# Kernel tuning notes

Hardware: AMD Instinct MI355X
Metric: run time of the kernel (lower is better)

The kernel has to match this reference:

```python
import jax, jax.numpy as jnp
import numpy as np

OUT_DIM = 64
NUM_HEADS = 8
HID = NUM_HEADS * OUT_DIM  # 512
ALPHA = 0.01  # leaky relu slope
N_NODES = 20000
N_EDGES = 100000
MP_LEN = 3


def setup_inputs() -> dict:
    key = jax.random.key(0)
    ks = jax.random.split(key, 8)
    s = 1.0 / np.sqrt(HID)
    return {
        "features": jax.random.normal(ks[0], (N_NODES, OUT_DIM), jnp.float32),
        "W_ih": jax.random.normal(ks[1], (3 * HID, OUT_DIM), jnp.float32) * s,
        "W_hh": jax.random.normal(ks[2], (3 * HID, HID), jnp.float32) * s,
        "b_ih": jax.random.normal(ks[3], (3 * HID,), jnp.float32) * s,
        "b_hh": jax.random.normal(ks[4], (3 * HID,), jnp.float32) * s,
        "attn": jax.random.normal(ks[5], (NUM_HEADS, OUT_DIM), jnp.float32) * 0.1,
        "edge_metapath_indices": jax.random.randint(ks[6], (N_EDGES, MP_LEN), 0, N_NODES),
        "edge_dst": jax.random.randint(ks[7], (N_EDGES,), 0, N_NODES),
    }


def _gru_last_hidden(x_seq, W_ih, W_hh, b_ih, b_hh):
    """x_seq: [L, E, D] -> final hidden [E, HID] (torch nn.GRU math, h0=0)."""
    E = x_seq.shape[1]
    h0 = jnp.zeros((E, HID), x_seq.dtype)

    def step(h, x):
        gi = x @ W_ih.T + b_ih  # [E, 3*HID]
        gh = h @ W_hh.T + b_hh  # [E, 3*HID]
        i_r, i_z, i_n = jnp.split(gi, 3, axis=-1)
        h_r, h_z, h_n = jnp.split(gh, 3, axis=-1)
        r = jax.nn.sigmoid(i_r + h_r)
        z = jax.nn.sigmoid(i_z + h_z)
        n = jnp.tanh(i_n + r * h_n)
        h_new = (1.0 - z) * n + z * h
        return h_new, None

    h_last, _ = jax.lax.scan(step, h0, x_seq)
    return h_last


def reference(features, W_ih, W_hh, b_ih, b_hh, attn,
              edge_metapath_indices, edge_dst):
    N = features.shape[0]
    # gather metapath node features: [E, L, D] -> GRU over L
    edata = features[edge_metapath_indices]
    h = _gru_last_hidden(jnp.transpose(edata, (1, 0, 2)), W_ih, W_hh, b_ih, b_hh)
    eft = h.reshape(-1, NUM_HEADS, OUT_DIM)  # [E, H, D]
    # attention logits per edge/head + leaky relu
    a = jnp.sum(eft * attn[None], axis=-1)  # [E, H]
    a = jnp.where(a >= 0, a, ALPHA * a)
    # edge softmax grouped by destination node
    amax = jax.ops.segment_max(a, edge_dst, num_segments=N)  # [N, H]
    ea = jnp.exp(a - amax[edge_dst])
    denom = jax.ops.segment_sum(ea, edge_dst, num_segments=N)  # [N, H]
    alpha = ea / denom[edge_dst]  # [E, H]
    # weighted message aggregation (sum) to destination nodes
    msg = eft * alpha[:, :, None]  # [E, H, D]
    ret = jax.ops.segment_sum(msg, edge_dst, num_segments=N)  # [N, H, D]
    return ret
```

## Files before the change

kernel.cpp:

```cpp
#include <hip/hip_runtime.h>
#include <hip/hip_bf16.h>

#define N_NODES 20000
#define N_EDGES 100000
#define HID 512
#define G3 1536
#define NH 8
#define OD 64

typedef __hip_bfloat16 bf16;
typedef __attribute__((ext_vector_type(8))) short bf16x8;
typedef __attribute__((ext_vector_type(4))) float f32x4;

__device__ __forceinline__ float frcp(float x) { return __builtin_amdgcn_rcpf(x); }
__device__ __forceinline__ float fsig(float x) { return frcp(1.0f + __expf(-x)); }
__device__ __forceinline__ float ftanh(float x) { return 1.0f - 2.0f * frcp(__expf(2.0f * x) + 1.0f); }
__device__ __forceinline__ float b2f(bf16 b) { return __bfloat162float(b); }
__device__ __forceinline__ bf16 f2b(float f) { return __float2bfloat16(f); }
__device__ __forceinline__ float bs2f(short s) {
    return __uint_as_float(((unsigned)(unsigned short)s) << 16);
}
__device__ __forceinline__ float us2f(unsigned short s) {
    return __uint_as_float(((unsigned)s) << 16);
}
__device__ __forceinline__ short f2bs(float f) {
    bf16 b = __float2bfloat16(f);
    return *reinterpret_cast<short*>(&b);
}
__device__ __forceinline__ unsigned ford(float f) {
    unsigned u = __float_as_uint(f);
    return (u & 0x80000000u) ? ~u : (u | 0x80000000u);
}
__device__ __forceinline__ float iford(unsigned u) {
    return __uint_as_float((u & 0x80000000u) ? (u & 0x7fffffffu) : ~u);
}

__device__ __forceinline__ void g2l16(const void* g, void* l) {
#if __has_builtin(__builtin_amdgcn_global_load_lds)
    __builtin_amdgcn_global_load_lds((const __attribute__((address_space(1))) char*)g,
                                     (__attribute__((address_space(3))) char*)l, 16, 0, 0);
#else
    *(bf16x8*)l = *(const bf16x8*)g;
#endif
}


__global__ __launch_bounds__(256) void k_prep(const float* __restrict__ Whh,
                                              const float* __restrict__ Wih,
                                              const float* __restrict__ feat,
                                              bf16* __restrict__ WTs,
                                              bf16* __restrict__ WIE,
                                              bf16* __restrict__ featB,
                                              float* __restrict__ WIT) {
    int t = blockIdx.x * 256 + threadIdx.x;
    if (t < 98304) {
        int T = t >> 10, c = (t >> 6) & 15, l = t & 63;
        int n = T * 16 + (l & 15);
        int k = c * 32 + ((l >> 4) << 3);
        const float* src = Whh + (size_t)n * 512 + k;
        bf16x8 v;
#pragma unroll
        for (int j = 0; j < 8; ++j) v[j] = f2bs(src[j]);
        *(bf16x8*)(WTs + (size_t)t * 8) = v;
    } else if (t < 196608) {
        int u = t - 98304;
        int d = u / 1536, j = u % 1536;
        WIT[u] = Wih[(size_t)j * 64 + d];
    } else if (t < 208896) {
        int u = t - 196608;
        int l = u & 63, cc = (u >> 6) & 1, jt = (u >> 7) & 31, g = u >> 12;
        int row = g * 512 + jt * 16 + (l & 15);
        int d0 = cc * 32 + ((l >> 4) << 3);
        const float* src = Wih + (size_t)row * 64 + d0;
        bf16x8 v;
#pragma unroll
        for (int j = 0; j < 8; ++j) v[j] = f2bs(src[j]);
        *(bf16x8*)(WIE + (size_t)u * 8) = v;
    } else {
        int u = t - 208896;
        const float* src = feat + (size_t)u * 8;
        bf16x8 v;
#pragma unroll
        for (int j = 0; j < 8; ++j) v[j] = f2bs(src[j]);
        *(bf16x8*)(featB + (size_t)u * 8) = v;
    }
}

__global__ __launch_bounds__(256) void k_count(const int* __restrict__ dst,
                                               unsigned* __restrict__ cnt) {
    int e = blockIdx.x * 256 + threadIdx.x;
    if (e < N_EDGES) atomicAdd(&cnt[dst[e]], 1u);
}

#define SCAN_CH 79
__global__ __launch_bounds__(256) void k_scan(const unsigned* __restrict__ cnt,
                                              unsigned* __restrict__ base,
                                              unsigned* __restrict__ cursor) {
    __shared__ unsigned ls[256];
    int t = threadIdx.x;
    int s0 = t * SCAN_CH;
    int s1 = s0 + SCAN_CH < N_NODES ? s0 + SCAN_CH : N_NODES;
    unsigned s = 0;
    for (int i = s0; i < s1; ++i) s += cnt[i];
    ls[t] = s;
    __syncthreads();
    for (int d = 1; d < 256; d <<= 1) {
        unsigned v = (t >= d) ? ls[t - d] : 0u;
        __syncthreads();
        ls[t] += v;
        __syncthreads();
    }
    unsigned run = ls[t] - s;
    for (int i = s0; i < s1; ++i) {
        base[i] = run; cursor[i] = run; run += cnt[i];
    }
    if (t == 255) base[N_NODES] = ls[255];
}

__global__ __launch_bounds__(256) void k_fill(const int* __restrict__ dst,
                                              unsigned* __restrict__ cursor,
                                              unsigned* __restrict__ csr) {
    int e = blockIdx.x * 256 + threadIdx.x;
    if (e < N_EDGES) {
        unsigned p = atomicAdd(&cursor[dst[e]], 1u);
        csr[p] = (unsigned)e;
    }
}

__global__ __launch_bounds__(256) void k_gi(const float* __restrict__ feat,
                                            const float* __restrict__ WIT,
                                            const float* __restrict__ b_ih,
                                            const float* __restrict__ b_hh,
                                            bf16* __restrict__ G,
                                            bf16* __restrict__ H1) {
    __shared__ float fs[16][64];
    const int n0 = blockIdx.x * 16;
    const int k = blockIdx.y * 256 + threadIdx.x;
    for (int i = threadIdx.x; i < 16 * 64; i += 256)
        fs[0][i] = feat[(size_t)n0 * 64 + i];
    __syncthreads();
    float acc[3][16];
#pragma unroll
    for (int g = 0; g < 3; ++g) {
        float b = b_ih[g * 512 + k];
#pragma unroll
        for (int e = 0; e < 16; ++e) acc[g][e] = b;
    }
    for (int d = 0; d < 64; d += 4) {
        float w[3][4];
#pragma unroll
        for (int u = 0; u < 4; ++u)
#pragma unroll
            for (int g = 0; g < 3; ++g)
                w[g][u] = WIT[(size_t)(d + u) * G3 + g * 512 + k];
#pragma unroll
        for (int e = 0; e < 16; ++e) {
            float4 f = *(const float4*)&fs[e][d];
#pragma unroll
            for (int g = 0; g < 3; ++g)
                acc[g][e] += w[g][0] * f.x + w[g][1] * f.y + w[g][2] * f.z + w[g][3] * f.w;
        }
    }
    const float br = b_hh[k], bz = b_hh[512 + k], bn = b_hh[1024 + k];
#pragma unroll
    for (int e = 0; e < 16; ++e) {
        bf16* dst = G + (size_t)(n0 + e) * G3 + k * 3;
        dst[0] = f2b(acc[0][e]);
        dst[1] = f2b(acc[1][e]);
        dst[2] = f2b(acc[2][e]);
        float r1 = fsig(acc[0][e] + br);
        float z1 = fsig(acc[1][e] + bz);
        float n1 = ftanh(acc[2][e] + r1 * bn);
        H1[(size_t)(n0 + e) * HID + k] = f2b((1.0f - z1) * n1);
    }
}

__global__ __launch_bounds__(256, 2) void k_gh2(const bf16* __restrict__ H1,
                                                const bf16* __restrict__ WTs,
                                                const float* __restrict__ b_hh,
                                                bf16* __restrict__ GH2) {
    __shared__ short Bs[2][8192];
    const int tid = threadIdx.x;
    const int wave = tid >> 6, lane = tid & 63;
    const int m0 = blockIdx.x * 128;
    const int k0 = (lane >> 4) << 3;

    bf16x8 afrag[2][16];
#pragma unroll
    for (int t = 0; t < 2; ++t) {
        int row = m0 + wave * 32 + t * 16 + (lane & 15);
        int ar = row < N_NODES ? row : N_NODES - 1;
#pragma unroll
        for (int c = 0; c < 16; ++c)
            afrag[t][c] = *(const bf16x8*)(H1 + (size_t)ar * HID + c * 32 + k0);
    }

    const int col = lane & 15;
    const int qb = (lane >> 4) << 2;
    const int boff = lane * 8;

#pragma unroll
    for (int i = 0; i < 4; ++i) {
        int q = tid + i * 256;
        g2l16(WTs + (size_t)q * 8, &Bs[0][q * 8]);
    }
    __syncthreads();

    int cur = 0;
    for (int jt = 0; jt < 32; ++jt) {
        const int cj = jt * 16 + col;
        f32x4 acc[2][3];
#pragma unroll
        for (int t = 0; t < 2; ++t)
#pragma unroll
            for (int g = 0; g < 3; ++g) acc[t][g] = (f32x4){0, 0, 0, 0};
        const float br = b_hh[cj], bz = b_hh[512 + cj], bn = b_hh[1024 + cj];
        {
#pragma unroll
            for (int i = 0; i < 4; ++i) {
                int q = tid + i * 256;
                g2l16(WTs + 262144 + (size_t)jt * 8192 + q * 8, &Bs[cur ^ 1][q * 8]);
            }
            const short* cb = &Bs[cur][0];
#pragma unroll
            for (int c = 0; c < 16; ++c) {
                bf16x8 b = *(const bf16x8*)&cb[c * 512 + boff];
                acc[0][0] = __builtin_amdgcn_mfma_f32_16x16x32_bf16(afrag[0][c], b, acc[0][0], 0, 0, 0);
                acc[1][0] = __builtin_amdgcn_mfma_f32_16x16x32_bf16(afrag[1][c], b, acc[1][0], 0, 0, 0);
            }
            __syncthreads();
            cur ^= 1;
        }
        {
#pragma unroll
            for (int i = 0; i < 4; ++i) {
                int q = tid + i * 256;
                g2l16(WTs + 524288 + (size_t)jt * 8192 + q * 8, &Bs[cur ^ 1][q * 8]);
            }
            const short* cb = &Bs[cur][0];
#pragma unroll
            for (int c = 0; c < 16; ++c) {
                bf16x8 b = *(const bf16x8*)&cb[c * 512 + boff];
                acc[0][1] = __builtin_amdgcn_mfma_f32_16x16x32_bf16(afrag[0][c], b, acc[0][1], 0, 0, 0);
                acc[1][1] = __builtin_amdgcn_mfma_f32_16x16x32_bf16(afrag[1][c], b, acc[1][1], 0, 0, 0);
            }
            __syncthreads();
            cur ^= 1;
        }
        {
            if (jt < 31) {
#pragma unroll
                for (int i = 0; i < 4; ++i) {
                    int q = tid + i * 256;
                    g2l16(WTs + (size_t)(jt + 1) * 8192 + q * 8, &Bs[cur ^ 1][q * 8]);
                }
            }
            const short* cb = &Bs[cur][0];
#pragma unroll
            for (int c = 0; c < 16; ++c) {
                bf16x8 b = *(const bf16x8*)&cb[c * 512 + boff];
                acc[0][2] = __builtin_amdgcn_mfma_f32_16x16x32_bf16(afrag[0][c], b, acc[0][2], 0, 0, 0);
                acc[1][2] = __builtin_amdgcn_mfma_f32_16x16x32_bf16(afrag[1][c], b, acc[1][2], 0, 0, 0);
            }
#pragma unroll
            for (int t = 0; t < 2; ++t)
#pragma unroll
                for (int q = 0; q < 4; ++q) {
                    int e = m0 + wave * 32 + t * 16 + qb + q;
                    if (e < N_NODES) {
                        bf16* dst = GH2 + (size_t)e * G3 + cj * 3;
                        dst[0] = f2b(acc[t][0][q] + br);
                        dst[1] = f2b(acc[t][1][q] + bz);
                        dst[2] = f2b(acc[t][2][q] + bn);
                    }
                }
            __syncthreads();
            cur ^= 1;
        }
    }
}

__global__ __launch_bounds__(256) void k_h2(const bf16* __restrict__ G,
                                            const bf16* __restrict__ GH2,
                                            const bf16* __restrict__ H1,
                                            const int* __restrict__ emi,
                                            bf16* __restrict__ h2) {
    size_t i = (size_t)blockIdx.x * 256 + threadIdx.x;
    int e = (int)(i >> 6);
    int kc = (int)(i & 63) * 8;
    int i0 = emi[(size_t)e * 3 + 0];
    int i1 = emi[(size_t)e * 3 + 1];
    const bf16* g1p = G + (size_t)i1 * G3 + kc * 3;
    const bf16* ghp = GH2 + (size_t)i0 * G3 + kc * 3;
    bf16x8 h1v = *(const bf16x8*)(H1 + (size_t)i0 * HID + kc);
    short s1[24], sh[24];
    {
        bf16x8 a0 = *(const bf16x8*)g1p, a1 = *(const bf16x8*)(g1p + 8), a2 = *(const bf16x8*)(g1p + 16);
        bf16x8 c0 = *(const bf16x8*)ghp, c1 = *(const bf16x8*)(ghp + 8), c2 = *(const bf16x8*)(ghp + 16);
#pragma unroll
        for (int j = 0; j < 8; ++j) {
            s1[j] = a0[j]; s1[8 + j] = a1[j]; s1[16 + j] = a2[j];
            sh[j] = c0[j]; sh[8 + j] = c1[j]; sh[16 + j] = c2[j];
        }
    }
    bf16x8 out;
#pragma unroll
    for (int j = 0; j < 8; ++j) {
        float r = fsig(bs2f(s1[j * 3 + 0]) + bs2f(sh[j * 3 + 0]));
        float z = fsig(bs2f(s1[j * 3 + 1]) + bs2f(sh[j * 3 + 1]));
        float n = ftanh(bs2f(s1[j * 3 + 2]) + r * bs2f(sh[j * 3 + 2]));
        out[j] = f2bs((1.0f - z) * n + z * bs2f(h1v[j]));
    }
    *(bf16x8*)(h2 + (size_t)e * HID + kc) = out;
}

__global__ __launch_bounds__(256, 3) void k_gemm3(const bf16* __restrict__ featB,
                                                  const bf16* __restrict__ WTs,
                                                  const bf16* __restrict__ WIE,
                                                  const float* __restrict__ b_ih,
                                                  const float* __restrict__ b_hh,
                                                  const int* __restrict__ emi,
                                                  bf16* __restrict__ h2) {
    __shared__ short Bs[2][9216];
    __shared__ int si2[64];
    const int tid = threadIdx.x;
    const int wave = tid >> 6, lane = tid & 63;
    const int m0 = blockIdx.x * 64;
    if (tid < 64) {
        int e = m0 + tid;
        si2[tid] = emi[(size_t)(e < N_EDGES ? e : N_EDGES - 1) * 3 + 2];
    }
    const int k0 = (lane >> 4) << 3;
    const int col = lane & 15;
    const int qb = (lane >> 4) << 2;
    const int boff = lane * 8;

#pragma unroll
    for (int i = 0; i < 4; ++i) {
        int q = tid + i * 256;
        g2l16(WTs + (size_t)q * 8, &Bs[0][q * 8]);
    }
    if (tid < 128) g2l16(WIE + (size_t)tid * 8, &Bs[0][8192 + tid * 8]);
    __syncthreads();

    bf16x8 afrag[18];
    {
        int row = m0 + wave * 16 + (lane & 15);
        int ar = row < N_EDGES ? row : N_EDGES - 1;
#pragma unroll
        for (int c = 0; c < 16; ++c)
            afrag[c] = *(const bf16x8*)(h2 + (size_t)ar * HID + c * 32 + k0);
        int i2r = si2[wave * 16 + (lane & 15)];
        afrag[16] = *(const bf16x8*)(featB + (size_t)i2r * 64 + k0);
        afrag[17] = *(const bf16x8*)(featB + (size_t)i2r * 64 + 32 + k0);
    }

    int cur = 0;
    for (int jt = 0; jt < 32; ++jt) {
        const int cj = jt * 16 + col;
        f32x4 ar_ = {0, 0, 0, 0}, az_ = {0, 0, 0, 0};
        f32x4 ahn = {0, 0, 0, 0}, ain = {0, 0, 0, 0};
        float bihr, bihz, bihn, bhhr, bhhz, bhhn;
        unsigned short ph[4];
        {
            bihr = b_ih[cj]; bihz = b_ih[512 + cj]; bihn = b_ih[1024 + cj];
            bhhr = b_hh[cj]; bhhz = b_hh[512 + cj]; bhhn = b_hh[1024 + cj];
#pragma unroll
            for (int q = 0; q < 4; ++q) {
                int e = m0 + wave * 16 + qb + q;
                int ec = e < N_EDGES ? e : N_EDGES - 1;
                ph[q] = ((const unsigned short*)h2)[(size_t)ec * HID + cj];
            }
#pragma unroll
            for (int i = 0; i < 4; ++i) {
                int q = tid + i * 256;
                g2l16(WTs + 262144 + (size_t)jt * 8192 + q * 8, &Bs[cur ^ 1][q * 8]);
            }
            if (tid < 128)
                g2l16(WIE + 32768 + (size_t)jt * 1024 + tid * 8, &Bs[cur ^ 1][8192 + tid * 8]);
            const short* cb = &Bs[cur][0];
#pragma unroll
            for (int c = 0; c < 16; ++c) {
                bf16x8 b = *(const bf16x8*)&cb[c * 512 + boff];
                ar_ = __builtin_amdgcn_mfma_f32_16x16x32_bf16(afrag[c], b, ar_, 0, 0, 0);
            }
            {
                bf16x8 b16 = *(const bf16x8*)&cb[8192 + boff];
                bf16x8 b17 = *(const bf16x8*)&cb[8192 + 512 + boff];
                ar_ = __builtin_amdgcn_mfma_f32_16x16x32_bf16(afrag[16], b16, ar_, 0, 0, 0);
                ar_ = __builtin_amdgcn_mfma_f32_16x16x32_bf16(afrag[17], b17, ar_, 0, 0, 0);
            }
            __syncthreads();
            cur ^= 1;
        }
        {
#pragma unroll
            for (int i = 0; i < 4; ++i) {
                int q = tid + i * 256;
                g2l16(WTs + 524288 + (size_t)jt * 8192 + q * 8, &Bs[cur ^ 1][q * 8]);
            }
            if (tid < 128)
                g2l16(WIE + 65536 + (size_t)jt * 1024 + tid * 8, &Bs[cur ^ 1][8192 + tid * 8]);
            const short* cb = &Bs[cur][0];
#pragma unroll
            for (int c = 0; c < 16; ++c) {
                bf16x8 b = *(const bf16x8*)&cb[c * 512 + boff];
                az_ = __builtin_amdgcn_mfma_f32_16x16x32_bf16(afrag[c], b, az_, 0, 0, 0);
            }
            {
                bf16x8 b16 = *(const bf16x8*)&cb[8192 + boff];
                bf16x8 b17 = *(const bf16x8*)&cb[8192 + 512 + boff];
                az_ = __builtin_amdgcn_mfma_f32_16x16x32_bf16(afrag[16], b16, az_, 0, 0, 0);
                az_ = __builtin_amdgcn_mfma_f32_16x16x32_bf16(afrag[17], b17, az_, 0, 0, 0);
            }
            __syncthreads();
            cur ^= 1;
        }
        {
            if (jt < 31) {
#pragma unroll
                for (int i = 0; i < 4; ++i) {
                    int q = tid + i * 256;
                    g2l16(WTs + (size_t)(jt + 1) * 8192 + q * 8, &Bs[cur ^ 1][q * 8]);
                }
                if (tid < 128)
                    g2l16(WIE + (size_t)(jt + 1) * 1024 + tid * 8, &Bs[cur ^ 1][8192 + tid * 8]);
            }
            const short* cb = &Bs[cur][0];
#pragma unroll
            for (int c = 0; c < 16; ++c) {
                bf16x8 b = *(const bf16x8*)&cb[c * 512 + boff];
                ahn = __builtin_amdgcn_mfma_f32_16x16x32_bf16(afrag[c], b, ahn, 0, 0, 0);
            }
            {
                bf16x8 b16 = *(const bf16x8*)&cb[8192 + boff];
                bf16x8 b17 = *(const bf16x8*)&cb[8192 + 512 + boff];
                ain = __builtin_amdgcn_mfma_f32_16x16x32_bf16(afrag[16], b16, ain, 0, 0, 0);
                ain = __builtin_amdgcn_mfma_f32_16x16x32_bf16(afrag[17], b17, ain, 0, 0, 0);
            }
#pragma unroll
            for (int q = 0; q < 4; ++q) {
                int e = m0 + wave * 16 + qb + q;
                if (e < N_EDGES) {
                    float r = fsig(ar_[q] + bihr + bhhr);
                    float z = fsig(az_[q] + bihz + bhhz);
                    float n = ftanh(ain[q] + bihn + r * (ahn[q] + bhhn));
                    h2[(size_t)e * HID + cj] = f2b((1.0f - z) * n + z * us2f(ph[q]));
                }
            }
            __syncthreads();
            cur ^= 1;
        }
    }
}

__global__ __launch_bounds__(256) void k_logits(const bf16* __restrict__ eft,
                                                const float* __restrict__ attn,
                                                const int* __restrict__ dst,
                                                float* __restrict__ a,
                                                unsigned* __restrict__ amax) {
    int i = blockIdx.x * 256 + threadIdx.x;
    int e = i >> 3, h = i & 7;
    const __hip_bfloat162* f2 = (const __hip_bfloat162*)(eft + (size_t)e * HID + h * OD);
    const float* at = attn + h * OD;
    float s = 0.f;
#pragma unroll
    for (int d = 0; d < OD / 2; ++d) {
        float2 fv = __bfloat1622float2(f2[d]);
        s += fv.x * at[2 * d] + fv.y * at[2 * d + 1];
    }
    s = (s >= 0.f) ? s : 0.01f * s;
    a[i] = s;
    atomicMax(&amax[(size_t)dst[e] * NH + h], ford(s));
}

__global__ __launch_bounds__(256) void k_ea(const int* __restrict__ dst,
                                            const unsigned* __restrict__ amax,
                                            float* __restrict__ a,
                                            float* __restrict__ denom) {
    int i = blockIdx.x * 256 + threadIdx.x;
    int e = i >> 3, h = i & 7;
    float m = iford(amax[(size_t)dst[e] * NH + h]);
    float v = __expf(a[i] - m);
    a[i] = v;
    atomicAdd(&denom[(size_t)dst[e] * NH + h], v);
}

__global__ __launch_bounds__(256) void k_out(const bf16* __restrict__ eft,
                                             const float* __restrict__ a,
                                             const float* __restrict__ denom,
                                             const unsigned* __restrict__ base,
                                             const unsigned* __restrict__ csr,
                                             float* __restrict__ out) {
    int n = blockIdx.x;
    int k = blockIdx.y * 256 + threadIdx.x;
    int h = k >> 6;
    unsigned b0 = base[n], b1 = base[n + 1];
    float rden = (b1 > b0) ? frcp(denom[(size_t)n * NH + h]) : 0.0f;
    float acc = 0.f;
    for (unsigned i = b0; i < b1; ++i) {
        unsigned e = csr[i];
        float al = a[(size_t)e * NH + h];
        acc += b2f(eft[(size_t)e * HID + k]) * al;
    }
    out[(size_t)n * HID + k] = acc * rden;
}

extern "C" void kernel_launch(void* const* d_in, const int* in_sizes, int n_in,
                              void* d_out, int out_size, void* d_ws, size_t ws_size,
                              hipStream_t stream) {
    (void)in_sizes; (void)n_in; (void)ws_size; (void)out_size;
    const float* feat = (const float*)d_in[0];
    const float* W_ih = (const float*)d_in[1];
    const float* W_hh = (const float*)d_in[2];
    const float* b_ih = (const float*)d_in[3];
    const float* b_hh = (const float*)d_in[4];
    const float* attn = (const float*)d_in[5];
    const int* emi = (const int*)d_in[6];
    const int* dst = (const int*)d_in[7];
    float* out = (float*)d_out;

    char* ws = (char*)d_ws;
    bf16* G = (bf16*)ws;
    bf16* GH2 = (bf16*)(ws + 61440000);
    bf16* h2 = (bf16*)(ws + 122880000);
    bf16* WTs = (bf16*)(ws + 225280000);
    float* WIT = (float*)(ws + 226852864);
    float* a = (float*)(ws + 227246080);
    unsigned* amax = (unsigned*)(ws + 230446080);
    float* denom = (float*)(ws + 231086080);
    unsigned* cnt = (unsigned*)(ws + 231726080);
    unsigned* base = (unsigned*)(ws + 231806080);
    unsigned* cursor = (unsigned*)(ws + 231886088);
    unsigned* csr = (unsigned*)(ws + 231966088);
    bf16* H1 = (bf16*)(ws + 232366088);
    bf16* WIE = (bf16*)(ws + 227246080);
    bf16* featB = (bf16*)(ws + 227442688);

    (void)hipMemsetAsync(amax, 0, 1360000, stream);

    k_prep<<<1441, 256, 0, stream>>>(W_hh, W_ih, feat, WTs, WIE, featB, WIT);
    k_count<<<391, 256, 0, stream>>>(dst, cnt);
    k_scan<<<1, 256, 0, stream>>>(cnt, base, cursor);
    k_fill<<<391, 256, 0, stream>>>(dst, cursor, csr);
    k_gi<<<dim3(1250, 2), 256, 0, stream>>>(feat, WIT, b_ih, b_hh, G, H1);
    k_gh2<<<157, 256, 0, stream>>>(H1, WTs, b_hh, GH2);
    k_h2<<<25000, 256, 0, stream>>>(G, GH2, H1, emi, h2);
    k_gemm3<<<1563, 256, 0, stream>>>(featB, WTs, WIE, b_ih, b_hh, emi, h2);
    k_logits<<<3125, 256, 0, stream>>>(h2, attn, dst, a, amax);
    k_ea<<<3125, 256, 0, stream>>>(dst, amax, a, denom);
    k_out<<<dim3(N_NODES, 2), 256, 0, stream>>>(h2, a, denom, base, csr, out);
}
```

Measured before the change: 788.6 us.

## Triple-buffer gate weight tiles in GRU step-3 GEMM with explicit waitcnt pipelining

Replaces the double-buffered LDS staging in k_gemm3 with three buffers, one per gate (r, z, n). Each gate's weights are prefetched two stages ahead, and the full __syncthreads is replaced by s_waitcnt vmcnt plus s_barrier. The WIE layout is padded so every thread issues one uniform 16-byte load per stage, and s_setprio is raised around the MFMA bursts. Launch bounds drop from 3 to 2 blocks per CU to fit the larger LDS footprint, which trades occupancy for deeper prefetch.

```diff
diff --git a/kernel.cpp b/kernel.cpp
--- a/kernel.cpp
+++ b/kernel.cpp
@@ -49,7 +49,7 @@
                                               const float* __restrict__ Wih,
                                               const float* __restrict__ feat,
                                               bf16* __restrict__ WTs,
-                                              bf16* __restrict__ WIE,
+                                              bf16* __restrict__ WIEp,
                                               bf16* __restrict__ featB,
                                               float* __restrict__ WIT) {
     int t = blockIdx.x * 256 + threadIdx.x;
@@ -68,14 +68,15 @@
         WIT[u] = Wih[(size_t)j * 64 + d];
     } else if (t < 208896) {
         int u = t - 196608;
-        int l = u & 63, cc = (u >> 6) & 1, jt = (u >> 7) & 31, g = u >> 12;
+        int q = u & 127, jt = (u >> 7) & 31, g = u >> 12;
+        int l = q & 63, cc = (q >> 6) & 1;
         int row = g * 512 + jt * 16 + (l & 15);
         int d0 = cc * 32 + ((l >> 4) << 3);
         const float* src = Wih + (size_t)row * 64 + d0;
         bf16x8 v;
 #pragma unroll
         for (int j = 0; j < 8; ++j) v[j] = f2bs(src[j]);
-        *(bf16x8*)(WIE + (size_t)u * 8) = v;
+        *(bf16x8*)(WIEp + ((size_t)g * 32 + jt) * 2048 + q * 8) = v;
     } else {
         int u = t - 208896;
         const float* src = feat + (size_t)u * 8;
@@ -314,14 +315,14 @@
     *(bf16x8*)(h2 + (size_t)e * HID + kc) = out;
 }
 
-__global__ __launch_bounds__(256, 3) void k_gemm3(const bf16* __restrict__ featB,
+__global__ __launch_bounds__(256, 2) void k_gemm3(const bf16* __restrict__ featB,
                                                   const bf16* __restrict__ WTs,
-                                                  const bf16* __restrict__ WIE,
+                                                  const bf16* __restrict__ WIEp,
                                                   const float* __restrict__ b_ih,
                                                   const float* __restrict__ b_hh,
                                                   const int* __restrict__ emi,
                                                   bf16* __restrict__ h2) {
-    __shared__ short Bs[2][9216];
+    __shared__ short Bs[3][10240];
     __shared__ int si2[64];
     const int tid = threadIdx.x;
     const int wave = tid >> 6, lane = tid & 63;
@@ -335,13 +336,22 @@
     const int qb = (lane >> 4) << 2;
     const int boff = lane * 8;
 
-#pragma unroll
-    for (int i = 0; i < 4; ++i) {
-        int q = tid + i * 256;
-        g2l16(WTs + (size_t)q * 8, &Bs[0][q * 8]);
-    }
-    if (tid < 128) g2l16(WIE + (size_t)tid * 8, &Bs[0][8192 + tid * 8]);
-    __syncthreads();
+#define STAGE_G3(gg, jj, bb) do {                                                   \
+        _Pragma("unroll")                                                           \
+        for (int i_ = 0; i_ < 4; ++i_) {                                            \
+            int q_ = tid + i_ * 256;                                                \
+            g2l16(WTs + (size_t)(gg) * 262144 + (size_t)(jj) * 8192 + q_ * 8,       \
+                  &Bs[bb][q_ * 8]);                                                 \
+        }                                                                           \
+        g2l16(WIEp + ((size_t)(gg) * 32 + (jj)) * 2048 + tid * 8,                   \
+              &Bs[bb][8192 + tid * 8]);                                             \
+    } while (0)
+
+    STAGE_G3(0, 0, 0);
+    STAGE_G3(1, 0, 1);
+    asm volatile("s_waitcnt vmcnt(5) lgkmcnt(0)" ::: "memory");
+    __builtin_amdgcn_s_barrier();
+    __builtin_amdgcn_sched_barrier(0);
 
     bf16x8 afrag[18];
     {
@@ -355,7 +365,6 @@
         afrag[17] = *(const bf16x8*)(featB + (size_t)i2r * 64 + 32 + k0);
     }
 
-    int cur = 0;
     for (int jt = 0; jt < 32; ++jt) {
         const int cj = jt * 16 + col;
         f32x4 ar_ = {0, 0, 0, 0}, az_ = {0, 0, 0, 0};
@@ -363,6 +372,10 @@
         float bihr, bihz, bihn, bhhr, bhhz, bhhn;
         unsigned short ph[4];
         {
+            asm volatile("s_waitcnt vmcnt(5)" ::: "memory");
+            __builtin_amdgcn_s_barrier();
+            __builtin_amdgcn_sched_barrier(0);
+            STAGE_G3(2, jt, 2);
             bihr = b_ih[cj]; bihz = b_ih[512 + cj]; bihn = b_ih[1024 + cj];
             bhhr = b_hh[cj]; bhhz = b_hh[512 + cj]; bhhn = b_hh[1024 + cj];
 #pragma unroll
@@ -371,14 +384,8 @@
                 int ec = e < N_EDGES ? e : N_EDGES - 1;
                 ph[q] = ((const unsigned short*)h2)[(size_t)ec * HID + cj];
             }
-#pragma unroll
-            for (int i = 0; i < 4; ++i) {
-                int q = tid + i * 256;
-                g2l16(WTs + 262144 + (size_t)jt * 8192 + q * 8, &Bs[cur ^ 1][q * 8]);
-            }
-            if (tid < 128)
-                g2l16(WIE + 32768 + (size_t)jt * 1024 + tid * 8, &Bs[cur ^ 1][8192 + tid * 8]);
-            const short* cb = &Bs[cur][0];
+            const short* cb = &Bs[0][0];
+            __builtin_amdgcn_s_setprio(1);
 #pragma unroll
             for (int c = 0; c < 16; ++c) {
                 bf16x8 b = *(const bf16x8*)&cb[c * 512 + boff];
@@ -386,22 +393,19 @@
             }
             {
                 bf16x8 b16 = *(const bf16x8*)&cb[8192 + boff];
-                bf16x8 b17 = *(const bf16x8*)&cb[8192 + 512 + boff];
+                bf16x8 b17 = *(const bf16x8*)&cb[8704 + boff];
                 ar_ = __builtin_amdgcn_mfma_f32_16x16x32_bf16(afrag[16], b16, ar_, 0, 0, 0);
                 ar_ = __builtin_amdgcn_mfma_f32_16x16x32_bf16(afrag[17], b17, ar_, 0, 0, 0);
             }
-            __syncthreads();
-            cur ^= 1;
+            __builtin_amdgcn_s_setprio(0);
         }
         {
-#pragma unroll
-            for (int i = 0; i < 4; ++i) {
-                int q = tid + i * 256;
-                g2l16(WTs + 524288 + (size_t)jt * 8192 + q * 8, &Bs[cur ^ 1][q * 8]);
-            }
-            if (tid < 128)
-                g2l16(WIE + 65536 + (size_t)jt * 1024 + tid * 8, &Bs[cur ^ 1][8192 + tid * 8]);
-            const short* cb = &Bs[cur][0];
+            asm volatile("s_waitcnt vmcnt(5)" ::: "memory");
+            __builtin_amdgcn_s_barrier();
+            __builtin_amdgcn_sched_barrier(0);
+            if (jt < 31) STAGE_G3(0, jt + 1, 0);
+            const short* cb = &Bs[1][0];
+            __builtin_amdgcn_s_setprio(1);
 #pragma unroll
             for (int c = 0; c < 16; ++c) {
                 bf16x8 b = *(const bf16x8*)&cb[c * 512 + boff];
@@ -409,24 +413,23 @@
             }
             {
                 bf16x8 b16 = *(const bf16x8*)&cb[8192 + boff];
-                bf16x8 b17 = *(const bf16x8*)&cb[8192 + 512 + boff];
+                bf16x8 b17 = *(const bf16x8*)&cb[8704 + boff];
                 az_ = __builtin_amdgcn_mfma_f32_16x16x32_bf16(afrag[16], b16, az_, 0, 0, 0);
                 az_ = __builtin_amdgcn_mfma_f32_16x16x32_bf16(afrag[17], b17, az_, 0, 0, 0);
             }
-            __syncthreads();
-            cur ^= 1;
+            __builtin_amdgcn_s_setprio(0);
         }
         {
             if (jt < 31) {
-#pragma unroll
-                for (int i = 0; i < 4; ++i) {
-                    int q = tid + i * 256;
-                    g2l16(WTs + (size_t)(jt + 1) * 8192 + q * 8, &Bs[cur ^ 1][q * 8]);
-                }
-                if (tid < 128)
-                    g2l16(WIE + (size_t)(jt + 1) * 1024 + tid * 8, &Bs[cur ^ 1][8192 + tid * 8]);
-            }
-            const short* cb = &Bs[cur][0];
+                asm volatile("s_waitcnt vmcnt(5)" ::: "memory");
+            } else {
+                asm volatile("s_waitcnt vmcnt(0)" ::: "memory");
+            }
+            __builtin_amdgcn_s_barrier();
+            __builtin_amdgcn_sched_barrier(0);
+            if (jt < 31) STAGE_G3(1, jt + 1, 1);
+            const short* cb = &Bs[2][0];
+            __builtin_amdgcn_s_setprio(1);
 #pragma unroll
             for (int c = 0; c < 16; ++c) {
                 bf16x8 b = *(const bf16x8*)&cb[c * 512 + boff];
@@ -434,10 +437,11 @@
             }
             {
                 bf16x8 b16 = *(const bf16x8*)&cb[8192 + boff];
-                bf16x8 b17 = *(const bf16x8*)&cb[8192 + 512 + boff];
+                bf16x8 b17 = *(const bf16x8*)&cb[8704 + boff];
                 ain = __builtin_amdgcn_mfma_f32_16x16x32_bf16(afrag[16], b16, ain, 0, 0, 0);
                 ain = __builtin_amdgcn_mfma_f32_16x16x32_bf16(afrag[17], b17, ain, 0, 0, 0);
             }
+            __builtin_amdgcn_s_setprio(0);
 #pragma unroll
             for (int q = 0; q < 4; ++q) {
                 int e = m0 + wave * 16 + qb + q;
@@ -448,10 +452,9 @@
                     h2[(size_t)e * HID + cj] = f2b((1.0f - z) * n + z * us2f(ph[q]));
                 }
             }
-            __syncthreads();
-            cur ^= 1;
-        }
-    }
+        }
+    }
+#undef STAGE_G3
 }
 
 __global__ __launch_bounds__(256) void k_logits(const bf16* __restrict__ eft,
@@ -534,19 +537,19 @@
     unsigned* cursor = (unsigned*)(ws + 231886088);
     unsigned* csr = (unsigned*)(ws + 231966088);
     bf16* H1 = (bf16*)(ws + 232366088);
-    bf16* WIE = (bf16*)(ws + 227246080);
-    bf16* featB = (bf16*)(ws + 227442688);
+    bf16* WIEp = (bf16*)(ws + 227246080);
+    bf16* featB = (bf16*)(ws + 227639296);
 
     (void)hipMemsetAsync(amax, 0, 1360000, stream);
 
-    k_prep<<<1441, 256, 0, stream>>>(W_hh, W_ih, feat, WTs, WIE, featB, WIT);
+    k_prep<<<1441, 256, 0, stream>>>(W_hh, W_ih, feat, WTs, WIEp, featB, WIT);
     k_count<<<391, 256, 0, stream>>>(dst, cnt);
     k_scan<<<1, 256, 0, stream>>>(cnt, base, cursor);
     k_fill<<<391, 256, 0, stream>>>(dst, cursor, csr);
     k_gi<<<dim3(1250, 2), 256, 0, stream>>>(feat, WIT, b_ih, b_hh, G, H1);
     k_gh2<<<157, 256, 0, stream>>>(H1, WTs, b_hh, GH2);
     k_h2<<<25000, 256, 0, stream>>>(G, GH2, H1, emi, h2);
-    k_gemm3<<<1563, 256, 0, stream>>>(featB, WTs, WIE, b_ih, b_hh, emi, h2);
+    k_gemm3<<<1563, 256, 0, stream>>>(featB, WTs, WIEp, b_ih, b_hh, emi, h2);
     k_logits<<<3125, 256, 0, stream>>>(h2, attn, dst, a, amax);
     k_ea<<<3125, 256, 0, stream>>>(dst, amax, a, denom);
     k_out<<<dim3(N_NODES, 2), 256, 0, stream>>>(h2, a, denom, base, csr, out);
```

After: 804.5 us. 1.02x slower.

## Stage GRU output tiles in LDS for coalesced vector stores

Applied to the files above, without the earlier changes.

The GH2 kernel now collects each column tile's gate pre-activations in shared memory and writes them to global memory as 16-byte rows on the next iteration. Before this it issued scattered 2-byte stores. The final GRU step kernel loads previous-hidden tiles into LDS with async copies, updates them in place, and writes back 64-column chunks with vector stores. It also precomputes the combined biases once per block in LDS. This targets uncoalesced narrow global loads and stores, at the cost of extra LDS use, which may lower occupancy, and more synchronisation around the tile buffer.

```diff
diff --git a/kernel.cpp b/kernel.cpp
--- a/kernel.cpp
+++ b/kernel.cpp
@@ -68,7 +68,8 @@
         WIT[u] = Wih[(size_t)j * 64 + d];
     } else if (t < 208896) {
         int u = t - 196608;
-        int l = u & 63, cc = (u >> 6) & 1, jt = (u >> 7) & 31, g = u >> 12;
+        int l = u & 63, cc = (u >> 6) & 1, jg = u >> 7;
+        int jt = jg & 31, g = jg >> 5;
         int row = g * 512 + jt * 16 + (l & 15);
         int d0 = cc * 32 + ((l >> 4) << 3);
         const float* src = Wih + (size_t)row * 64 + d0;
@@ -180,6 +181,7 @@
                                                 const float* __restrict__ b_hh,
                                                 bf16* __restrict__ GH2) {
     __shared__ short Bs[2][8192];
+    __shared__ short tile2[128 * 48];
     const int tid = threadIdx.x;
     const int wave = tid >> 6, lane = tid & 63;
     const int m0 = blockIdx.x * 128;
@@ -216,6 +218,17 @@
             for (int g = 0; g < 3; ++g) acc[t][g] = (f32x4){0, 0, 0, 0};
         const float br = b_hh[cj], bz = b_hh[512 + cj], bn = b_hh[1024 + cj];
         {
+            if (jt > 0) {
+                int pj = jt - 1;
+#pragma unroll
+                for (int i_ = 0; i_ < 3; ++i_) {
+                    int idx = i_ * 256 + tid;
+                    int rg = m0 + (idx / 6);
+                    if (rg < N_NODES)
+                        *(bf16x8*)(GH2 + (size_t)rg * G3 + pj * 48 + (idx % 6) * 8) =
+                            *(const bf16x8*)&tile2[idx * 8];
+                }
+            }
 #pragma unroll
             for (int i = 0; i < 4; ++i) {
                 int q = tid + i * 256;
@@ -266,17 +279,23 @@
             for (int t = 0; t < 2; ++t)
 #pragma unroll
                 for (int q = 0; q < 4; ++q) {
-                    int e = m0 + wave * 32 + t * 16 + qb + q;
-                    if (e < N_NODES) {
-                        bf16* dst = GH2 + (size_t)e * G3 + cj * 3;
-                        dst[0] = f2b(acc[t][0][q] + br);
-                        dst[1] = f2b(acc[t][1][q] + bz);
-                        dst[2] = f2b(acc[t][2][q] + bn);
-                    }
+                    int lr = wave * 32 + t * 16 + qb + q;
+                    short* s = &tile2[lr * 48 + col * 3];
+                    s[0] = f2bs(acc[t][0][q] + br);
+                    s[1] = f2bs(acc[t][1][q] + bz);
+                    s[2] = f2bs(acc[t][2][q] + bn);
                 }
             __syncthreads();
             cur ^= 1;
         }
+    }
+#pragma unroll
+    for (int i_ = 0; i_ < 3; ++i_) {
+        int idx = i_ * 256 + tid;
+        int rg = m0 + (idx / 6);
+        if (rg < N_NODES)
+            *(bf16x8*)(GH2 + (size_t)rg * G3 + 31 * 48 + (idx % 6) * 8) =
+                *(const bf16x8*)&tile2[idx * 8];
     }
 }
 
@@ -322,6 +341,8 @@
                                                   const int* __restrict__ emi,
                                                   bf16* __restrict__ h2) {
     __shared__ short Bs[2][9216];
+    __shared__ short tile[64 * 64];
+    __shared__ float bias4[2048];
     __shared__ int si2[64];
     const int tid = threadIdx.x;
     const int wave = tid >> 6, lane = tid & 63;
@@ -330,17 +351,44 @@
         int e = m0 + tid;
         si2[tid] = emi[(size_t)(e < N_EDGES ? e : N_EDGES - 1) * 3 + 2];
     }
+#pragma unroll
+    for (int j = 0; j < 8; ++j) {
+        int idx = j * 256 + tid;
+        int arr = idx >> 9, c = idx & 511;
+        float v;
+        if (arr == 0) v = b_ih[c] + b_hh[c];
+        else if (arr == 1) v = b_ih[512 + c] + b_hh[512 + c];
+        else if (arr == 2) v = b_ih[1024 + c];
+        else v = b_hh[1024 + c];
+        bias4[idx] = v;
+    }
     const int k0 = (lane >> 4) << 3;
     const int col = lane & 15;
     const int qb = (lane >> 4) << 2;
     const int boff = lane * 8;
 
-#pragma unroll
-    for (int i = 0; i < 4; ++i) {
-        int q = tid + i * 256;
-        g2l16(WTs + (size_t)q * 8, &Bs[0][q * 8]);
-    }
-    if (tid < 128) g2l16(WIE + (size_t)tid * 8, &Bs[0][8192 + tid * 8]);
+#define STAGE_W(gg, jj) do {                                                        \
+        _Pragma("unroll")                                                           \
+        for (int i_ = 0; i_ < 4; ++i_) {                                            \
+            int q_ = tid + i_ * 256;                                                \
+            g2l16(WTs + (size_t)(gg) * 262144 + (size_t)(jj) * 8192 + q_ * 8,       \
+                  &Bs[cur ^ 1][q_ * 8]);                                            \
+        }                                                                           \
+        if (tid < 128)                                                              \
+            g2l16(WIE + (size_t)(gg) * 32768 + (size_t)(jj) * 1024 + tid * 8,       \
+                  &Bs[cur ^ 1][8192 + tid * 8]);                                    \
+    } while (0)
+
+    {
+        int cur = 1;
+        STAGE_W(0, 0);
+    }
+#pragma unroll
+    for (int i_ = 0; i_ < 2; ++i_) {
+        int idx = i_ * 256 + tid;
+        int rg = m0 + (idx >> 3); if (rg >= N_EDGES) rg = N_EDGES - 1;
+        g2l16(h2 + (size_t)rg * HID + (idx & 7) * 8, &tile[idx * 8]);
+    }
     __syncthreads();
 
     bf16x8 afrag[18];
@@ -360,24 +408,8 @@
         const int cj = jt * 16 + col;
         f32x4 ar_ = {0, 0, 0, 0}, az_ = {0, 0, 0, 0};
         f32x4 ahn = {0, 0, 0, 0}, ain = {0, 0, 0, 0};
-        float bihr, bihz, bihn, bhhr, bhhz, bhhn;
-        unsigned short ph[4];
         {
-            bihr = b_ih[cj]; bihz = b_ih[512 + cj]; bihn = b_ih[1024 + cj];
-            bhhr = b_hh[cj]; bhhz = b_hh[512 + cj]; bhhn = b_hh[1024 + cj];
-#pragma unroll
-            for (int q = 0; q < 4; ++q) {
-                int e = m0 + wave * 16 + qb + q;
-                int ec = e < N_EDGES ? e : N_EDGES - 1;
-                ph[q] = ((const unsigned short*)h2)[(size_t)ec * HID + cj];
-            }
-#pragma unroll
-            for (int i = 0; i < 4; ++i) {
-                int q = tid + i * 256;
-                g2l16(WTs + 262144 + (size_t)jt * 8192 + q * 8, &Bs[cur ^ 1][q * 8]);
-            }
-            if (tid < 128)
-                g2l16(WIE + 32768 + (size_t)jt * 1024 + tid * 8, &Bs[cur ^ 1][8192 + tid * 8]);
+            STAGE_W(1, jt);
             const short* cb = &Bs[cur][0];
 #pragma unroll
             for (int c = 0; c < 16; ++c) {
@@ -386,7 +418,7 @@
             }
             {
                 bf16x8 b16 = *(const bf16x8*)&cb[8192 + boff];
-                bf16x8 b17 = *(const bf16x8*)&cb[8192 + 512 + boff];
+                bf16x8 b17 = *(const bf16x8*)&cb[8704 + boff];
                 ar_ = __builtin_amdgcn_mfma_f32_16x16x32_bf16(afrag[16], b16, ar_, 0, 0, 0);
                 ar_ = __builtin_amdgcn_mfma_f32_16x16x32_bf16(afrag[17], b17, ar_, 0, 0, 0);
             }
@@ -394,13 +426,7 @@
             cur ^= 1;
         }
         {
-#pragma unroll
-            for (int i = 0; i < 4; ++i) {
-                int q = tid + i * 256;
-                g2l16(WTs + 524288 + (size_t)jt * 8192 + q * 8, &Bs[cur ^ 1][q * 8]);
-            }
-            if (tid < 128)
-                g2l16(WIE + 65536 + (size_t)jt * 1024 + tid * 8, &Bs[cur ^ 1][8192 + tid * 8]);
+            STAGE_W(2, jt);
             const short* cb = &Bs[cur][0];
 #pragma unroll
             for (int c = 0; c < 16; ++c) {
@@ -409,7 +435,7 @@
             }
             {
                 bf16x8 b16 = *(const bf16x8*)&cb[8192 + boff];
-                bf16x8 b17 = *(const bf16x8*)&cb[8192 + 512 + boff];
+                bf16x8 b17 = *(const bf16x8*)&cb[8704 + boff];
                 az_ = __builtin_amdgcn_mfma_f32_16x16x32_bf16(afrag[16], b16, az_, 0, 0, 0);
                 az_ = __builtin_amdgcn_mfma_f32_16x16x32_bf16(afrag[17], b17, az_, 0, 0, 0);
             }
@@ -417,15 +443,7 @@
             cur ^= 1;
         }
         {
-            if (jt < 31) {
-#pragma unroll
-                for (int i = 0; i < 4; ++i) {
-                    int q = tid + i * 256;
-                    g2l16(WTs + (size_t)(jt + 1) * 8192 + q * 8, &Bs[cur ^ 1][q * 8]);
-                }
-                if (tid < 128)
-                    g2l16(WIE + (size_t)(jt + 1) * 1024 + tid * 8, &Bs[cur ^ 1][8192 + tid * 8]);
-            }
+            if (jt < 31) STAGE_W(0, jt + 1);
             const short* cb = &Bs[cur][0];
 #pragma unroll
             for (int c = 0; c < 16; ++c) {
@@ -434,24 +452,51 @@
             }
             {
                 bf16x8 b16 = *(const bf16x8*)&cb[8192 + boff];
-                bf16x8 b17 = *(const bf16x8*)&cb[8192 + 512 + boff];
+                bf16x8 b17 = *(const bf16x8*)&cb[8704 + boff];
                 ain = __builtin_amdgcn_mfma_f32_16x16x32_bf16(afrag[16], b16, ain, 0, 0, 0);
                 ain = __builtin_amdgcn_mfma_f32_16x16x32_bf16(afrag[17], b17, ain, 0, 0, 0);
             }
-#pragma unroll
-            for (int q = 0; q < 4; ++q) {
-                int e = m0 + wave * 16 + qb + q;
-                if (e < N_EDGES) {
-                    float r = fsig(ar_[q] + bihr + bhhr);
-                    float z = fsig(az_[q] + bihz + bhhz);
-                    float n = ftanh(ain[q] + bihn + r * (ahn[q] + bhhn));
-                    h2[(size_t)e * HID + cj] = f2b((1.0f - z) * n + z * us2f(ph[q]));
+            {
+                const float rb = bias4[cj], zb = bias4[512 + cj];
+                const float nb = bias4[1024 + cj], hb = bias4[1536 + cj];
+                const int tc = ((jt & 3) << 4) + col;
+#pragma unroll
+                for (int q = 0; q < 4; ++q) {
+                    int lrow = wave * 16 + qb + q;
+                    short* slot = &tile[lrow * 64 + tc];
+                    float phv = bs2f(*slot);
+                    float r = fsig(ar_[q] + rb);
+                    float z = fsig(az_[q] + zb);
+                    float n = ftanh(ain[q] + nb + r * (ahn[q] + hb));
+                    *slot = f2bs((1.0f - z) * n + z * phv);
                 }
             }
             __syncthreads();
             cur ^= 1;
-        }
-    }
+            if ((jt & 3) == 3) {
+                const int g4 = jt >> 2;
+#pragma unroll
+                for (int i_ = 0; i_ < 2; ++i_) {
+                    int idx = i_ * 256 + tid;
+                    int rg = m0 + (idx >> 3);
+                    if (rg < N_EDGES)
+                        *(bf16x8*)(h2 + (size_t)rg * HID + g4 * 64 + (idx & 7) * 8) =
+                            *(const bf16x8*)&tile[idx * 8];
+                }
+                __builtin_amdgcn_sched_barrier(0);
+                if (jt < 31) {
+#pragma unroll
+                    for (int i_ = 0; i_ < 2; ++i_) {
+                        int idx = i_ * 256 + tid;
+                        int rg = m0 + (idx >> 3); if (rg >= N_EDGES) rg = N_EDGES - 1;
+                        g2l16(h2 + (size_t)rg * HID + (g4 + 1) * 64 + (idx & 7) * 8,
+                              &tile[idx * 8]);
+                    }
+                }
+            }
+        }
+    }
+#undef STAGE_W
 }
 
 __global__ __launch_bounds__(256) void k_logits(const bf16* __restrict__ eft,
```

Result: no change. 803.1 us (+1.8%).

## Fuse attention logits into GRU GEMM epilogue and softmax into aggregation

Applied to the files above, without the earlier changes.

Attention logit computation and the leaky-relu/atomicMax are folded into the k_gemm3 epilogue, using a per-head shuffle reduction of the hidden values times attn. The separate exp/denominator kernel is removed: k_out now recomputes exp(a-max) and the denominator on the fly while aggregating, with 512-thread blocks over the full hidden dim. k_gh2 is retiled to 64 rows per block with higher occupancy. This eliminates two launches and re-reading h2 for logits, at the cost of redundant exp work per thread in k_out and extra epilogue work in the GEMM.

```diff
diff --git a/kernel.cpp b/kernel.cpp
--- a/kernel.cpp
+++ b/kernel.cpp
@@ -68,7 +68,8 @@
         WIT[u] = Wih[(size_t)j * 64 + d];
     } else if (t < 208896) {
         int u = t - 196608;
-        int l = u & 63, cc = (u >> 6) & 1, jt = (u >> 7) & 31, g = u >> 12;
+        int l = u & 63, cc = (u >> 6) & 1, jg = u >> 7;
+        int jt = jg & 31, g = jg >> 5;
         int row = g * 512 + jt * 16 + (l & 15);
         int d0 = cc * 32 + ((l >> 4) << 3);
         const float* src = Wih + (size_t)row * 64 + d0;
@@ -175,24 +176,23 @@
     }
 }
 
-__global__ __launch_bounds__(256, 2) void k_gh2(const bf16* __restrict__ H1,
+__global__ __launch_bounds__(256, 4) void k_gh2(const bf16* __restrict__ H1,
                                                 const bf16* __restrict__ WTs,
                                                 const float* __restrict__ b_hh,
                                                 bf16* __restrict__ GH2) {
     __shared__ short Bs[2][8192];
     const int tid = threadIdx.x;
     const int wave = tid >> 6, lane = tid & 63;
-    const int m0 = blockIdx.x * 128;
+    const int m0 = blockIdx.x * 64;
     const int k0 = (lane >> 4) << 3;
 
-    bf16x8 afrag[2][16];
-#pragma unroll
-    for (int t = 0; t < 2; ++t) {
-        int row = m0 + wave * 32 + t * 16 + (lane & 15);
+    bf16x8 afrag[16];
+    {
+        int row = m0 + wave * 16 + (lane & 15);
         int ar = row < N_NODES ? row : N_NODES - 1;
 #pragma unroll
         for (int c = 0; c < 16; ++c)
-            afrag[t][c] = *(const bf16x8*)(H1 + (size_t)ar * HID + c * 32 + k0);
+            afrag[c] = *(const bf16x8*)(H1 + (size_t)ar * HID + c * 32 + k0);
     }
 
     const int col = lane & 15;
@@ -209,11 +209,7 @@
     int cur = 0;
     for (int jt = 0; jt < 32; ++jt) {
         const int cj = jt * 16 + col;
-        f32x4 acc[2][3];
-#pragma unroll
-        for (int t = 0; t < 2; ++t)
-#pragma unroll
-            for (int g = 0; g < 3; ++g) acc[t][g] = (f32x4){0, 0, 0, 0};
+        f32x4 a0 = {0, 0, 0, 0}, a1 = {0, 0, 0, 0}, a2 = {0, 0, 0, 0};
         const float br = b_hh[cj], bz = b_hh[512 + cj], bn = b_hh[1024 + cj];
         {
 #pragma unroll
@@ -225,8 +221,7 @@
 #pragma unroll
             for (int c = 0; c < 16; ++c) {
                 bf16x8 b = *(const bf16x8*)&cb[c * 512 + boff];
-                acc[0][0] = __builtin_amdgcn_mfma_f32_16x16x32_bf16(afrag[0][c], b, acc[0][0], 0, 0, 0);
-                acc[1][0] = __builtin_amdgcn_mfma_f32_16x16x32_bf16(afrag[1][c], b, acc[1][0], 0, 0, 0);
+                a0 = __builtin_amdgcn_mfma_f32_16x16x32_bf16(afrag[c], b, a0, 0, 0, 0);
             }
             __syncthreads();
             cur ^= 1;
@@ -241,8 +236,7 @@
 #pragma unroll
             for (int c = 0; c < 16; ++c) {
                 bf16x8 b = *(const bf16x8*)&cb[c * 512 + boff];
-                acc[0][1] = __builtin_amdgcn_mfma_f32_16x16x32_bf16(afrag[0][c], b, acc[0][1], 0, 0, 0);
-                acc[1][1] = __builtin_amdgcn_mfma_f32_16x16x32_bf16(afrag[1][c], b, acc[1][1], 0, 0, 0);
+                a1 = __builtin_amdgcn_mfma_f32_16x16x32_bf16(afrag[c], b, a1, 0, 0, 0);
             }
             __syncthreads();
             cur ^= 1;
@@ -259,21 +253,18 @@
 #pragma unroll
             for (int c = 0; c < 16; ++c) {
                 bf16x8 b = *(const bf16x8*)&cb[c * 512 + boff];
-                acc[0][2] = __builtin_amdgcn_mfma_f32_16x16x32_bf16(afrag[0][c], b, acc[0][2], 0, 0, 0);
-                acc[1][2] = __builtin_amdgcn_mfma_f32_16x16x32_bf16(afrag[1][c], b, acc[1][2], 0, 0, 0);
-            }
-#pragma unroll
-            for (int t = 0; t < 2; ++t)
-#pragma unroll
-                for (int q = 0; q < 4; ++q) {
-                    int e = m0 + wave * 32 + t * 16 + qb + q;
-                    if (e < N_NODES) {
-                        bf16* dst = GH2 + (size_t)e * G3 + cj * 3;
-                        dst[0] = f2b(acc[t][0][q] + br);
-                        dst[1] = f2b(acc[t][1][q] + bz);
-                        dst[2] = f2b(acc[t][2][q] + bn);
-                    }
+                a2 = __builtin_amdgcn_mfma_f32_16x16x32_bf16(afrag[c], b, a2, 0, 0, 0);
+            }
+#pragma unroll
+            for (int q = 0; q < 4; ++q) {
+                int e = m0 + wave * 16 + qb + q;
+                if (e < N_NODES) {
+                    bf16* dst = GH2 + (size_t)e * G3 + cj * 3;
+                    dst[0] = f2b(a0[q] + br);
+                    dst[1] = f2b(a1[q] + bz);
+                    dst[2] = f2b(a2[q] + bn);
                 }
+            }
             __syncthreads();
             cur ^= 1;
         }
@@ -320,16 +311,26 @@
                                                   const float* __restrict__ b_ih,
                                                   const float* __restrict__ b_hh,
                                                   const int* __restrict__ emi,
-                                                  bf16* __restrict__ h2) {
+                                                  const int* __restrict__ dst,
+                                                  const float* __restrict__ attn,
+                                                  bf16* __restrict__ h2,
+                                                  float* __restrict__ a,
+                                                  unsigned* __restrict__ amax) {
     __shared__ short Bs[2][9216];
     __shared__ int si2[64];
+    __shared__ int sdst[64];
+    __shared__ float As[512];
     const int tid = threadIdx.x;
     const int wave = tid >> 6, lane = tid & 63;
     const int m0 = blockIdx.x * 64;
     if (tid < 64) {
         int e = m0 + tid;
-        si2[tid] = emi[(size_t)(e < N_EDGES ? e : N_EDGES - 1) * 3 + 2];
-    }
+        int ec = e < N_EDGES ? e : N_EDGES - 1;
+        si2[tid] = emi[(size_t)ec * 3 + 2];
+        sdst[tid] = dst[ec];
+    }
+    As[tid] = attn[tid];
+    As[256 + tid] = attn[256 + tid];
     const int k0 = (lane >> 4) << 3;
     const int col = lane & 15;
     const int qb = (lane >> 4) << 2;
@@ -355,6 +356,7 @@
         afrag[17] = *(const bf16x8*)(featB + (size_t)i2r * 64 + 32 + k0);
     }
 
+    float hacc[4] = {0.f, 0.f, 0.f, 0.f};
     int cur = 0;
     for (int jt = 0; jt < 32; ++jt) {
         const int cj = jt * 16 + col;
@@ -438,15 +440,39 @@
                 ain = __builtin_amdgcn_mfma_f32_16x16x32_bf16(afrag[16], b16, ain, 0, 0, 0);
                 ain = __builtin_amdgcn_mfma_f32_16x16x32_bf16(afrag[17], b17, ain, 0, 0, 0);
             }
+            const float aw = As[cj];
 #pragma unroll
             for (int q = 0; q < 4; ++q) {
                 int e = m0 + wave * 16 + qb + q;
-                if (e < N_EDGES) {
-                    float r = fsig(ar_[q] + bihr + bhhr);
-                    float z = fsig(az_[q] + bihz + bhhz);
-                    float n = ftanh(ain[q] + bihn + r * (ahn[q] + bhhn));
-                    h2[(size_t)e * HID + cj] = f2b((1.0f - z) * n + z * us2f(ph[q]));
+                float r = fsig(ar_[q] + bihr + bhhr);
+                float z = fsig(az_[q] + bihz + bhhz);
+                float n = ftanh(ain[q] + bihn + r * (ahn[q] + bhhn));
+                float hv = (1.0f - z) * n + z * us2f(ph[q]);
+                hacc[q] += hv * aw;
+                if (e < N_EDGES) h2[(size_t)e * HID + cj] = f2b(hv);
+            }
+            if ((jt & 3) == 3) {
+                const int hd = jt >> 2;
+#pragma unroll
+                for (int m = 1; m < 16; m <<= 1) {
+#pragma unroll
+                    for (int q = 0; q < 4; ++q)
+                        hacc[q] += __shfl_xor(hacc[q], m, 64);
                 }
+                if ((lane & 15) == 0) {
+#pragma unroll
+                    for (int q = 0; q < 4; ++q) {
+                        int li = wave * 16 + qb + q;
+                        int e = m0 + li;
+                        if (e < N_EDGES) {
+                            float s = hacc[q];
+                            s = (s >= 0.f) ? s : 0.01f * s;
+                            a[(size_t)e * NH + hd] = s;
+                            atomicMax(&amax[(size_t)sdst[li] * NH + hd], ford(s));
+                        }
+                    }
+                }
+                hacc[0] = hacc[1] = hacc[2] = hacc[3] = 0.f;
             }
             __syncthreads();
             cur ^= 1;
@@ -454,56 +480,25 @@
     }
 }
 
-__global__ __launch_bounds__(256) void k_logits(const bf16* __restrict__ eft,
-                                                const float* __restrict__ attn,
-                                                const int* __restrict__ dst,
-                                                float* __restrict__ a,
-                                                unsigned* __restrict__ amax) {
-    int i = blockIdx.x * 256 + threadIdx.x;
-    int e = i >> 3, h = i & 7;
-    const __hip_bfloat162* f2 = (const __hip_bfloat162*)(eft + (size_t)e * HID + h * OD);
-    const float* at = attn + h * OD;
-    float s = 0.f;
-#pragma unroll
-    for (int d = 0; d < OD / 2; ++d) {
-        float2 fv = __bfloat1622float2(f2[d]);
-        s += fv.x * at[2 * d] + fv.y * at[2 * d + 1];
-    }
-    s = (s >= 0.f) ? s : 0.01f * s;
-    a[i] = s;
-    atomicMax(&amax[(size_t)dst[e] * NH + h], ford(s));
-}
-
-__global__ __launch_bounds__(256) void k_ea(const int* __restrict__ dst,
-                                            const unsigned* __restrict__ amax,
-                                            float* __restrict__ a,
-                                            float* __restrict__ denom) {
-    int i = blockIdx.x * 256 + threadIdx.x;
-    int e = i >> 3, h = i & 7;
-    float m = iford(amax[(size_t)dst[e] * NH + h]);
-    float v = __expf(a[i] - m);
-    a[i] = v;
-    atomicAdd(&denom[(size_t)dst[e] * NH + h], v);
-}
-
-__global__ __launch_bounds__(256) void k_out(const bf16* __restrict__ eft,
+__global__ __launch_bounds__(512) void k_out(const bf16* __restrict__ eft,
                                              const float* __restrict__ a,
-                                             const float* __restrict__ denom,
+                                             const unsigned* __restrict__ amax,
                                              const unsigned* __restrict__ base,
                                              const unsigned* __restrict__ csr,
                                              float* __restrict__ out) {
     int n = blockIdx.x;
-    int k = blockIdx.y * 256 + threadIdx.x;
+    int k = threadIdx.x;
     int h = k >> 6;
     unsigned b0 = base[n], b1 = base[n + 1];
-    float rden = (b1 > b0) ? frcp(denom[(size_t)n * NH + h]) : 0.0f;
-    float acc = 0.f;
+    float m = iford(amax[(size_t)n * NH + h]);
+    float acc = 0.f, dsum = 0.f;
     for (unsigned i = b0; i < b1; ++i) {
         unsigned e = csr[i];
-        float al = a[(size_t)e * NH + h];
-        acc += b2f(eft[(size_t)e * HID + k]) * al;
-    }
-    out[(size_t)n * HID + k] = acc * rden;
+        float ea = __expf(a[(size_t)e * NH + h] - m);
+        dsum += ea;
+        acc += b2f(eft[(size_t)e * HID + k]) * ea;
+    }
+    out[(size_t)n * HID + k] = (b1 > b0) ? acc * frcp(dsum) : 0.f;
 }
 
 extern "C" void kernel_launch(void* const* d_in, const int* in_sizes, int n_in,
@@ -526,9 +521,7 @@
     bf16* h2 = (bf16*)(ws + 122880000);
     bf16* WTs = (bf16*)(ws + 225280000);
     float* WIT = (float*)(ws + 226852864);
-    float* a = (float*)(ws + 227246080);
     unsigned* amax = (unsigned*)(ws + 230446080);
-    float* denom = (float*)(ws + 231086080);
     unsigned* cnt = (unsigned*)(ws + 231726080);
     unsigned* base = (unsigned*)(ws + 231806080);
     unsigned* cursor = (unsigned*)(ws + 231886088);
@@ -536,6 +529,7 @@
     bf16* H1 = (bf16*)(ws + 232366088);
     bf16* WIE = (bf16*)(ws + 227246080);
     bf16* featB = (bf16*)(ws + 227442688);
+    float* a = (float*)ws;
 
     (void)hipMemsetAsync(amax, 0, 1360000, stream);
 
@@ -544,10 +538,9 @@
     k_scan<<<1, 256, 0, stream>>>(cnt, base, cursor);
     k_fill<<<391, 256, 0, stream>>>(dst, cursor, csr);
     k_gi<<<dim3(1250, 2), 256, 0, stream>>>(feat, WIT, b_ih, b_hh, G, H1);
-    k_gh2<<<157, 256, 0, stream>>>(H1, WTs, b_hh, GH2);
+    k_gh2<<<313, 256, 0, stream>>>(H1, WTs, b_hh, GH2);
     k_h2<<<25000, 256, 0, stream>>>(G, GH2, H1, emi, h2);
-    k_gemm3<<<1563, 256, 0, stream>>>(featB, WTs, WIE, b_ih, b_hh, emi, h2);
-    k_logits<<<3125, 256, 0, stream>>>(h2, attn, dst, a, amax);
-    k_ea<<<3125, 256, 0, stream>>>(dst, amax, a, denom);
-    k_out<<<dim3(N_NODES, 2), 256, 0, stream>>>(h2, a, denom, base, csr, out);
-}
+    k_gemm3<<<1563, 256, 0, stream>>>(featB, WTs, WIE, b_ih, b_hh, emi, dst, attn,
+                                      h2, a, amax);
+    k_out<<<N_NODES, 512, 0, stream>>>(h2, a, amax, base, csr, out);
+}
```

Measured after the change: 793.5 us. About the same (+0.6%).
